# Performance work log

Hardware: AMD Instinct MI355X
Metric: run time of the kernel (lower is better)

The kernel has to match this reference:

```python
import jax, jax.numpy as jnp
import numpy as np


def setup_inputs() -> dict:
    key = jax.random.key(0)
    x = jax.random.normal(key, (4, 3, 8192), dtype=jnp.float32)  # (B, 3, N)
    return {"x": x, "k": 30}


def reference(x, k):
    # x: (B, 3, N)
    x_t = jnp.swapaxes(x, 1, 2)  # (B, N, 3)
    xx = jnp.sum(x_t ** 2, axis=2, keepdims=True)  # (B, N, 1)
    # pairwise squared distances (B, N, N)
    pairwise = xx + jnp.swapaxes(xx, 1, 2) - 2.0 * jnp.matmul(x_t, x)
    # k smallest distances -> negate and take top_k
    _, idx = jax.lax.top_k(-pairwise, k)  # idx: (B, N, k)
    # gather neighbors: (B, N, k, 3)
    neighbors = jax.vmap(lambda pts, i: pts[i])(x_t, idx)
    centroid = jnp.mean(neighbors, axis=2, keepdims=True)  # (B, N, 1, 3)
    centered = neighbors - centroid  # (B, N, k, 3)
    # per-point 3x3 covariance
    cov = jnp.einsum('bnki,bnkj->bnij', centered, centered)  # (B, N, 3, 3)
    _, v = jnp.linalg.eigh(cov)  # eigenvalues ascending
    normals = v[..., :, 0]  # eigenvector of smallest eigenvalue, (B, N, 3)
    # orient normals toward viewpoint (origin): view_dir = -x_t
    dot = jnp.sum(-x_t * normals, axis=-1, keepdims=True)
    normals = jnp.where(dot < 0, -normals, normals)
    x_out = jnp.concatenate([x, jnp.swapaxes(normals, 1, 2)], axis=1)  # (B, 6, N)
    return x_out
```

## Files before the change

### kernel.cpp

```cpp
#include <hip/hip_runtime.h>
#include <math.h>

#define N_PTS   8192
#define KNN     30
#define CAPG    104
#define STR     105
#define GROUPS  8
#define BLOCK   128
#define NZ      64
#define NY      64
#define NBKT    (NZ * NY)
#define CLO     -4.0f
#define CSC     8.0f
#define LAMBDA  48.0f

#define WS_S   0
#define WS_O   524288
#define WS_BS  655360
#define WS_GH  720912
#define WS_GC  786448

__device__ __forceinline__ int clampi(int v, int lo, int hi) {
    return v < lo ? lo : (v > hi ? hi : v);
}
__device__ __forceinline__ int bucket_of(float pz, float py) {
    int zb = clampi((int)floorf((pz - CLO) * CSC), 0, NZ - 1);
    int yb = clampi((int)floorf((py - CLO) * CSC), 0, NY - 1);
    return (zb << 6) | yb;
}

__global__ __launch_bounds__(256) void prep_hist_kernel(const float* __restrict__ x,
                                                        float* __restrict__ out,
                                                        int* __restrict__ ghist) {
    const int i = blockIdx.x * 256 + threadIdx.x;
    const int b = i >> 13;
    const int p = i & (N_PTS - 1);
    const float* xb = x + (size_t)b * 3 * N_PTS;
    float* ob = out + (size_t)b * 6 * N_PTS;
    float px = xb[p], py = xb[N_PTS + p], pz = xb[2 * N_PTS + p];
    ob[p]             = px;
    ob[N_PTS + p]     = py;
    ob[2 * N_PTS + p] = pz;
    atomicAdd(&ghist[(b << 12) + bucket_of(pz, py)], 1);
}

__global__ __launch_bounds__(1024) void prep_scan_kernel(const int* __restrict__ ghist,
                                                         int* __restrict__ bstart,
                                                         int* __restrict__ gcur) {
    __shared__ int wsum[16];
    const int b = blockIdx.x;
    const int t = threadIdx.x;
    const int wid = t >> 6, lane = t & 63;
    const int* gh = ghist + (b << 12);

    int l0 = gh[4 * t], l1 = gh[4 * t + 1], l2 = gh[4 * t + 2], l3 = gh[4 * t + 3];
    int s = l0 + l1 + l2 + l3;
    int sum = s;
    #pragma unroll
    for (int off = 1; off < 64; off <<= 1) {
        int v = __shfl_up(sum, off);
        if (lane >= off) sum += v;
    }
    if (lane == 63) wsum[wid] = sum;
    __syncthreads();
    if (t == 0) {
        int run = 0;
        #pragma unroll
        for (int k = 0; k < 16; ++k) { int v = wsum[k]; wsum[k] = run; run += v; }
    }
    __syncthreads();
    int base = wsum[wid] + (sum - s);
    int b0 = base, b1 = base + l0, b2 = b1 + l1, b3 = b2 + l2;
    int* bsb = bstart + b * (NBKT + 1);
    int* gc  = gcur + (b << 12);
    bsb[4 * t] = b0; bsb[4 * t + 1] = b1; bsb[4 * t + 2] = b2; bsb[4 * t + 3] = b3;
    gc[4 * t]  = b0; gc[4 * t + 1]  = b1; gc[4 * t + 2]  = b2; gc[4 * t + 3]  = b3;
    if (t == 1023) bsb[NBKT] = N_PTS;
}

__global__ __launch_bounds__(256) void prep_scatter_kernel(const float* __restrict__ x,
                                                           float4* __restrict__ S,
                                                           int* __restrict__ O,
                                                           int* __restrict__ gcur) {
    const int i = blockIdx.x * 256 + threadIdx.x;
    const int b = i >> 13;
    const int p = i & (N_PTS - 1);
    const float* xb = x + (size_t)b * 3 * N_PTS;
    float px = xb[p], py = xb[N_PTS + p], pz = xb[2 * N_PTS + p];
    int bk = bucket_of(pz, py);
    int dst = atomicAdd(&gcur[(b << 12) + bk], 1);
    float xx = __fadd_rn(__fadd_rn(__fmul_rn(px, px), __fmul_rn(py, py)),
                         __fmul_rn(pz, pz));
    S[((size_t)b << 13) + dst] = make_float4(px, py, pz, xx);
    O[((size_t)b << 13) + dst] = p;
}

__global__ __launch_bounds__(BLOCK, 6) void knn_normal_kernel(const float4* __restrict__ S,
                                                              const int* __restrict__ O,
                                                              const int* __restrict__ bstart,
                                                              float* __restrict__ out) {
    __shared__ unsigned long long ldk[GROUPS * STR];

    const int t    = threadIdx.x;
    const int l16  = t & 15;
    const int g    = t >> 4;
    const int gsh  = (t & 63) & ~15;
    const int qblk = (blockIdx.x * 1031) & 4095;
    const int qid  = qblk * GROUPS + g;
    const int b    = qid >> 13;
    const int pos  = qid & (N_PTS - 1);
    const float4* __restrict__ P  = S + ((size_t)b << 13);
    const int*    __restrict__ Ob = O + ((size_t)b << 13);
    const int*    __restrict__ bs = bstart + b * (NBKT + 1);
    const float4 qp = P[pos];
    const int    oi = Ob[pos];

    unsigned long long* __restrict__ ldg = ldk + g * STR;

    const float c = fmaxf(sqrtf(qp.w), 1e-3f);
    float rlo = 0.05f, rhi = 6.0f;
    for (int it = 0; it < 12; ++it) {
        float r = 0.5f * (rlo + rhi);
        float slo = fmaxf(c - r, 0.0f);
        float h = (c + r - slo) * 0.125f;
        float f = 0.0f;
        if (l16 <= 8) {
            float sq = slo + h * (float)l16;
            float cs = c - sq;
            float hh = fmaxf(fminf((r * r - cs * cs) * (0.5f / c), 2.0f * sq), 0.0f);
            float w = (l16 == 0 || l16 == 8) ? 1.0f : ((l16 & 1) ? 4.0f : 2.0f);
            f = w * __expf(-0.5f * sq * sq) * sq * hh;
        }
        f += __shfl_xor(f, 1, 16); f += __shfl_xor(f, 2, 16);
        f += __shfl_xor(f, 4, 16); f += __shfl_xor(f, 8, 16);
        float lam = 1089.3f * f * h;
        if (lam < LAMBDA) rlo = r; else rhi = r;
    }
    float rad = rhi * 1.02f;
    float r2  = rad * rad;

    int  cnt = 0;
    bool active = true;

    for (;;) {
        if (active) {
            cnt = 0;
            float w = __fmaf_rn(sqrtf(r2), 1.002f, 1e-3f);
            int zlo = clampi((int)floorf((qp.z - w - CLO) * CSC), 0, NZ - 1);
            int zhi = clampi((int)floorf((qp.z + w - CLO) * CSC), 0, NZ - 1);
            int ylo = clampi((int)floorf((qp.y - w - CLO) * CSC), 0, NY - 1);
            int yhi = clampi((int)floorf((qp.y + w - CLO) * CSC), 0, NY - 1);
            for (int zb = zlo; zb <= zhi; ++zb) {
                int lo = bs[(zb << 6) + ylo];
                int hi = bs[(zb << 6) + yhi + 1];
                int smax = (hi - lo + 31) >> 5;
                for (int s = 0; s < smax; ++s) {
                    int j1  = lo + (s << 5) + l16;
                    int j2  = j1 + 16;
                    int jc1 = j1 < hi ? j1 : hi - 1;
                    int jc2 = j2 < hi ? j2 : hi - 1;
                    float4 p1 = P[jc1];
                    float4 p2 = P[jc2];
                    float mm1 = __fmaf_rn(qp.z, p1.z, __fmaf_rn(qp.y, p1.y, __fmul_rn(qp.x, p1.x)));
                    float d1  = __fsub_rn(__fadd_rn(qp.w, p1.w), __fmul_rn(2.0f, mm1));
                    float mm2 = __fmaf_rn(qp.z, p2.z, __fmaf_rn(qp.y, p2.y, __fmul_rn(qp.x, p2.x)));
                    float d2  = __fsub_rn(__fadd_rn(qp.w, p2.w), __fmul_rn(2.0f, mm2));
                    bool hit1 = (j1 < hi) && (d1 <= r2);
                    bool hit2 = (j2 < hi) && (d2 <= r2);
                    unsigned long long m1 = __ballot(hit1);
                    unsigned sub1 = (unsigned)((m1 >> gsh) & 0xFFFFull);
                    if (hit1) {
                        int slot = cnt + __popc(sub1 & ((1u << l16) - 1u));
                        if (slot < CAPG) {
                            unsigned u = __float_as_uint(d1);
                            u = (u & 0x80000000u) ? ~u : (u | 0x80000000u);
                            ldg[slot] = ((unsigned long long)u << 28) | (unsigned long long)jc1;
                        }
                    }
                    cnt += __popc(sub1);
                    unsigned long long m2 = __ballot(hit2);
                    unsigned sub2 = (unsigned)((m2 >> gsh) & 0xFFFFull);
                    if (hit2) {
                        int slot = cnt + __popc(sub2 & ((1u << l16) - 1u));
                        if (slot < CAPG) {
                            unsigned u = __float_as_uint(d2);
                            u = (u & 0x80000000u) ? ~u : (u | 0x80000000u);
                            ldg[slot] = ((unsigned long long)u << 28) | (unsigned long long)jc2;
                        }
                    }
                    cnt += __popc(sub2);
                }
            }
        }
        bool bad = active && (cnt < KNN || cnt > CAPG);
        if (__ballot(bad) == 0ULL) break;
        active = bad;
        if (active) r2 = (cnt < KNN) ? r2 * 1.6f : r2 * 0.82f;
    }

    unsigned long long k0 = ~0ULL, k1 = ~0ULL, k2 = ~0ULL, k3 = ~0ULL,
                       k4 = ~0ULL, k5 = ~0ULL, k6 = ~0ULL;
    #define FILLK(J, KV) { int idx = l16 + 16 * (J); if (idx < cnt) {            \
        unsigned long long key = ldg[idx];                                       \
        int jc = (int)(key & 0x3FFFull);                                         \
        KV = (key & ~0x0FFFFFFFull) | ((unsigned long long)Ob[jc] << 14)         \
             | (unsigned long long)jc;                                           \
        ldg[idx] = KV; } }
    FILLK(0, k0) FILLK(1, k1) FILLK(2, k2) FILLK(3, k3)
    FILLK(4, k4) FILLK(5, k5) FILLK(6, k6)
    #undef FILLK
    __builtin_amdgcn_wave_barrier();

    int r0 = 0, r1 = 0, r2i = 0, r3 = 0, r4 = 0, r5 = 0, r6 = 0;
    if (cnt <= 64) {
        for (int u = 0; u < cnt; ++u) {
            unsigned long long ku = ldg[u];
            r0 += ku < k0; r1 += ku < k1; r2i += ku < k2; r3 += ku < k3;
        }
        r4 = r5 = r6 = KNN;
    } else {
        for (int u = 0; u < cnt; ++u) {
            unsigned long long ku = ldg[u];
            r0 += ku < k0; r1 += ku < k1; r2i += ku < k2; r3 += ku < k3;
            r4 += ku < k4; r5 += ku < k5; r6 += ku < k6;
        }
    }

    const double qx = (double)qp.x, qy = (double)qp.y, qz = (double)qp.z;
    double sx = 0.0, sy = 0.0, sz = 0.0;
    double sxx = 0.0, sxy = 0.0, sxz = 0.0, syy = 0.0, syz = 0.0, szz = 0.0;

    #define ACCJ(KV, RV) if ((RV) < KNN) {                                       \
        float4 p = P[(int)((KV) & 0x3FFFull)];                                   \
        double ax = (double)p.x - qx, ay = (double)p.y - qy, az = (double)p.z - qz; \
        sx += ax; sy += ay; sz += az;                                            \
        sxx = fma(ax, ax, sxx); sxy = fma(ax, ay, sxy); sxz = fma(ax, az, sxz);  \
        syy = fma(ay, ay, syy); syz = fma(ay, az, syz); szz = fma(az, az, szz); }
    ACCJ(k0, r0) ACCJ(k1, r1) ACCJ(k2, r2i) ACCJ(k3, r3)
    ACCJ(k4, r4) ACCJ(k5, r5) ACCJ(k6, r6)
    #undef ACCJ

    #pragma unroll
    for (int off = 1; off < 16; off <<= 1) {
        sx  += __shfl_xor(sx,  off, 16); sy  += __shfl_xor(sy,  off, 16); sz  += __shfl_xor(sz,  off, 16);
        sxx += __shfl_xor(sxx, off, 16); sxy += __shfl_xor(sxy, off, 16); sxz += __shfl_xor(sxz, off, 16);
        syy += __shfl_xor(syy, off, 16); syz += __shfl_xor(syz, off, 16); szz += __shfl_xor(szz, off, 16);
    }

    if (l16 == 0) {
        const double kinv = 1.0 / (double)KNN;
        double m00 = sxx - sx * sx * kinv;
        double m11 = syy - sy * sy * kinv;
        double m22 = szz - sz * sz * kinv;
        double m01 = sxy - sx * sy * kinv;
        double m02 = sxz - sx * sz * kinv;
        double m12 = syz - sy * sz * kinv;

        double nx = 1.0, ny = 0.0, nz = 0.0;
        double q3 = (m00 + m11 + m22) / 3.0;
        double p1 = m01 * m01 + m02 * m02 + m12 * m12;
        double d00 = m00 - q3, d11 = m11 - q3, d22 = m22 - q3;
        double p2 = d00 * d00 + d11 * d11 + d22 * d22 + 2.0 * p1;
        if (p2 > 1e-280) {
            double pp = sqrt(p2 / 6.0);
            double ip = 1.0 / pp;
            double b00 = d00 * ip, b11 = d11 * ip, b22 = d22 * ip;
            double b01 = m01 * ip, b02 = m02 * ip, b12 = m12 * ip;
            double detB = b00 * (b11 * b22 - b12 * b12)
                        - b01 * (b01 * b22 - b12 * b02)
                        + b02 * (b01 * b12 - b11 * b02);
            double rr = 0.5 * detB;
            rr = rr < -1.0 ? -1.0 : (rr > 1.0 ? 1.0 : rr);
            double phi = acos(rr) / 3.0;
            double lam = q3 + 2.0 * pp * cos(phi + 2.0943951023931953);
            double a00 = m00 - lam, a11 = m11 - lam, a22 = m22 - lam;
            double v0x = m01 * m12 - m02 * a11, v0y = m02 * m01 - a00 * m12, v0z = a00 * a11 - m01 * m01;
            double v1x = m01 * a22 - m02 * m12, v1y = m02 * m02 - a00 * a22, v1z = a00 * m12 - m01 * m02;
            double v2x = a11 * a22 - m12 * m12, v2y = m12 * m02 - m01 * a22, v2z = m01 * m12 - a11 * m02;
            double n0 = v0x * v0x + v0y * v0y + v0z * v0z;
            double n1 = v1x * v1x + v1y * v1y + v1z * v1z;
            double n2 = v2x * v2x + v2y * v2y + v2z * v2z;
            double bx = v0x, by = v0y, bz = v0z, bn = n0;
            if (n1 > bn) { bx = v1x; by = v1y; bz = v1z; bn = n1; }
            if (n2 > bn) { bx = v2x; by = v2y; bz = v2z; bn = n2; }
            if (bn > 1e-280) {
                double inv = 1.0 / sqrt(bn);
                nx = bx * inv; ny = by * inv; nz = bz * inv;
            }
        }
        double dq = -(qx * nx + qy * ny + qz * nz);
        if (dq < 0.0) { nx = -nx; ny = -ny; nz = -nz; }

        float* ob = out + (size_t)b * 6 * N_PTS;
        ob[3 * N_PTS + oi] = (float)nx;
        ob[4 * N_PTS + oi] = (float)ny;
        ob[5 * N_PTS + oi] = (float)nz;
    }
}

extern "C" void kernel_launch(void* const* d_in, const int* in_sizes, int n_in,
                              void* d_out, int out_size, void* d_ws, size_t ws_size,
                              hipStream_t stream) {
    const float* x = (const float*)d_in[0];
    float* out = (float*)d_out;
    char* ws = (char*)d_ws;
    float4* S    = (float4*)(ws + WS_S);
    int*    O    = (int*)(ws + WS_O);
    int*    bsta = (int*)(ws + WS_BS);
    int*    gh   = (int*)(ws + WS_GH);
    int*    gc   = (int*)(ws + WS_GC);

    hipMemsetAsync(gh, 0, 4 * NBKT * sizeof(int), stream);
    prep_hist_kernel   <<<dim3(128), dim3(256),  0, stream>>>(x, out, gh);
    prep_scan_kernel   <<<dim3(4),   dim3(1024), 0, stream>>>(gh, bsta, gc);
    prep_scatter_kernel<<<dim3(128), dim3(256),  0, stream>>>(x, S, O, gc);
    knn_normal_kernel  <<<dim3(32768 / GROUPS), dim3(BLOCK), 0, stream>>>(S, O, bsta, out);
}
```

Measured before the change: 170.9 us.

## Defer heavy KNN queries to a separate full-wave kernel

Before searching, each query estimates how many candidates its bucket window holds. Queries above a threshold are appended to a global list and handled by a second kernel that uses a full 64-lane wave per query instead of 16 lanes. This targets load imbalance, where a few dense queries hold up their waves. The bisection now runs 14 iterations instead of 12, and the unrolled fixed-register rank selection is replaced by a strided loop with a block-wide __syncthreads. The change adds an atomic-append pass, an extra kernel launch and a memset, and the deferred-list workspace reuses the region used by the histogram buffers.

```diff
diff --git a/kernel.cpp b/kernel.cpp
--- a/kernel.cpp
+++ b/kernel.cpp
@@ -13,12 +13,16 @@
 #define CLO     -4.0f
 #define CSC     8.0f
 #define LAMBDA  48.0f
+#define THRESH  1024
+#define HGRID   2048
 
 #define WS_S   0
 #define WS_O   524288
 #define WS_BS  655360
 #define WS_GH  720912
 #define WS_GC  786448
+#define WS_DL  720912
+#define WS_DC  851984
 
 __device__ __forceinline__ int clampi(int v, int lo, int hi) {
     return v < lo ? lo : (v > hi ? hi : v);
@@ -27,6 +31,81 @@
     int zb = clampi((int)floorf((pz - CLO) * CSC), 0, NZ - 1);
     int yb = clampi((int)floorf((py - CLO) * CSC), 0, NY - 1);
     return (zb << 6) | yb;
+}
+
+__device__ __forceinline__ float solve_r2(float qw, int l16) {
+    const float c = fmaxf(sqrtf(qw), 1e-3f);
+    float rlo = 0.05f, rhi = 6.0f;
+    for (int it = 0; it < 14; ++it) {
+        float r = 0.5f * (rlo + rhi);
+        float slo = fmaxf(c - r, 0.0f);
+        float h = (c + r - slo) * 0.125f;
+        float f = 0.0f;
+        if (l16 <= 8) {
+            float sq = slo + h * (float)l16;
+            float cs = c - sq;
+            float hh = fmaxf(fminf((r * r - cs * cs) * (0.5f / c), 2.0f * sq), 0.0f);
+            float w = (l16 == 0 || l16 == 8) ? 1.0f : ((l16 & 1) ? 4.0f : 2.0f);
+            f = w * __expf(-0.5f * sq * sq) * sq * hh;
+        }
+        f += __shfl_xor(f, 1, 16); f += __shfl_xor(f, 2, 16);
+        f += __shfl_xor(f, 4, 16); f += __shfl_xor(f, 8, 16);
+        float lam = 1089.3f * f * h;
+        if (lam < LAMBDA) rlo = r; else rhi = r;
+    }
+    float rad = rhi * 1.02f;
+    return rad * rad;
+}
+
+__device__ __forceinline__ void normal_epilogue(double sx, double sy, double sz,
+        double sxx, double sxy, double sxz, double syy, double syz, double szz,
+        double qx, double qy, double qz, float* ob, int oi) {
+    const double kinv = 1.0 / (double)KNN;
+    double m00 = sxx - sx * sx * kinv;
+    double m11 = syy - sy * sy * kinv;
+    double m22 = szz - sz * sz * kinv;
+    double m01 = sxy - sx * sy * kinv;
+    double m02 = sxz - sx * sz * kinv;
+    double m12 = syz - sy * sz * kinv;
+
+    double nx = 1.0, ny = 0.0, nz = 0.0;
+    double q3 = (m00 + m11 + m22) / 3.0;
+    double p1 = m01 * m01 + m02 * m02 + m12 * m12;
+    double d00 = m00 - q3, d11 = m11 - q3, d22 = m22 - q3;
+    double p2 = d00 * d00 + d11 * d11 + d22 * d22 + 2.0 * p1;
+    if (p2 > 1e-280) {
+        double pp = sqrt(p2 / 6.0);
+        double ip = 1.0 / pp;
+        double b00 = d00 * ip, b11 = d11 * ip, b22 = d22 * ip;
+        double b01 = m01 * ip, b02 = m02 * ip, b12 = m12 * ip;
+        double detB = b00 * (b11 * b22 - b12 * b12)
+                    - b01 * (b01 * b22 - b12 * b02)
+                    + b02 * (b01 * b12 - b11 * b02);
+        double rr = 0.5 * detB;
+        rr = rr < -1.0 ? -1.0 : (rr > 1.0 ? 1.0 : rr);
+        double phi = acos(rr) / 3.0;
+        double lam = q3 + 2.0 * pp * cos(phi + 2.0943951023931953);
+        double a00 = m00 - lam, a11 = m11 - lam, a22 = m22 - lam;
+        double v0x = m01 * m12 - m02 * a11, v0y = m02 * m01 - a00 * m12, v0z = a00 * a11 - m01 * m01;
+        double v1x = m01 * a22 - m02 * m12, v1y = m02 * m02 - a00 * a22, v1z = a00 * m12 - m01 * m02;
+        double v2x = a11 * a22 - m12 * m12, v2y = m12 * m02 - m01 * a22, v2z = m01 * m12 - a11 * m02;
+        double n0 = v0x * v0x + v0y * v0y + v0z * v0z;
+        double n1 = v1x * v1x + v1y * v1y + v1z * v1z;
+        double n2 = v2x * v2x + v2y * v2y + v2z * v2z;
+        double bx = v0x, by = v0y, bz = v0z, bn = n0;
+        if (n1 > bn) { bx = v1x; by = v1y; bz = v1z; bn = n1; }
+        if (n2 > bn) { bx = v2x; by = v2y; bz = v2z; bn = n2; }
+        if (bn > 1e-280) {
+            double inv = 1.0 / sqrt(bn);
+            nx = bx * inv; ny = by * inv; nz = bz * inv;
+        }
+    }
+    double dq = -(qx * nx + qy * ny + qz * nz);
+    if (dq < 0.0) { nx = -nx; ny = -ny; nz = -nz; }
+
+    ob[3 * N_PTS + oi] = (float)nx;
+    ob[4 * N_PTS + oi] = (float)ny;
+    ob[5 * N_PTS + oi] = (float)nz;
 }
 
 __global__ __launch_bounds__(256) void prep_hist_kernel(const float* __restrict__ x,
@@ -98,6 +177,8 @@
 __global__ __launch_bounds__(BLOCK, 6) void knn_normal_kernel(const float4* __restrict__ S,
                                                               const int* __restrict__ O,
                                                               const int* __restrict__ bstart,
+                                                              int* __restrict__ dlist,
+                                                              int* __restrict__ dcount,
                                                               float* __restrict__ out) {
     __shared__ unsigned long long ldk[GROUPS * STR];
 
@@ -117,30 +198,27 @@
 
     unsigned long long* __restrict__ ldg = ldk + g * STR;
 
-    const float c = fmaxf(sqrtf(qp.w), 1e-3f);
-    float rlo = 0.05f, rhi = 6.0f;
-    for (int it = 0; it < 12; ++it) {
-        float r = 0.5f * (rlo + rhi);
-        float slo = fmaxf(c - r, 0.0f);
-        float h = (c + r - slo) * 0.125f;
-        float f = 0.0f;
-        if (l16 <= 8) {
-            float sq = slo + h * (float)l16;
-            float cs = c - sq;
-            float hh = fmaxf(fminf((r * r - cs * cs) * (0.5f / c), 2.0f * sq), 0.0f);
-            float w = (l16 == 0 || l16 == 8) ? 1.0f : ((l16 & 1) ? 4.0f : 2.0f);
-            f = w * __expf(-0.5f * sq * sq) * sq * hh;
-        }
-        f += __shfl_xor(f, 1, 16); f += __shfl_xor(f, 2, 16);
-        f += __shfl_xor(f, 4, 16); f += __shfl_xor(f, 8, 16);
-        float lam = 1089.3f * f * h;
-        if (lam < LAMBDA) rlo = r; else rhi = r;
-    }
-    float rad = rhi * 1.02f;
-    float r2  = rad * rad;
+    float r2 = solve_r2(qp.w, l16);
+
+    bool defer;
+    {
+        float w = __fmaf_rn(sqrtf(r2), 1.002f, 1e-3f);
+        int zlo = clampi((int)floorf((qp.z - w - CLO) * CSC), 0, NZ - 1);
+        int zhi = clampi((int)floorf((qp.z + w - CLO) * CSC), 0, NZ - 1);
+        int ylo = clampi((int)floorf((qp.y - w - CLO) * CSC), 0, NY - 1);
+        int yhi = clampi((int)floorf((qp.y + w - CLO) * CSC), 0, NY - 1);
+        int tot = 0;
+        for (int zb = zlo; zb <= zhi; ++zb)
+            tot += bs[(zb << 6) + yhi + 1] - bs[(zb << 6) + ylo];
+        defer = tot > THRESH;
+    }
+    if (defer && l16 == 0) {
+        int slot = atomicAdd(dcount, 1);
+        dlist[slot] = qid;
+    }
 
     int  cnt = 0;
-    bool active = true;
+    bool active = !defer;
 
     for (;;) {
         if (active) {
@@ -198,47 +276,29 @@
         if (active) r2 = (cnt < KNN) ? r2 * 1.6f : r2 * 0.82f;
     }
 
-    unsigned long long k0 = ~0ULL, k1 = ~0ULL, k2 = ~0ULL, k3 = ~0ULL,
-                       k4 = ~0ULL, k5 = ~0ULL, k6 = ~0ULL;
-    #define FILLK(J, KV) { int idx = l16 + 16 * (J); if (idx < cnt) {            \
-        unsigned long long key = ldg[idx];                                       \
-        int jc = (int)(key & 0x3FFFull);                                         \
-        KV = (key & ~0x0FFFFFFFull) | ((unsigned long long)Ob[jc] << 14)         \
-             | (unsigned long long)jc;                                           \
-        ldg[idx] = KV; } }
-    FILLK(0, k0) FILLK(1, k1) FILLK(2, k2) FILLK(3, k3)
-    FILLK(4, k4) FILLK(5, k5) FILLK(6, k6)
-    #undef FILLK
-    __builtin_amdgcn_wave_barrier();
-
-    int r0 = 0, r1 = 0, r2i = 0, r3 = 0, r4 = 0, r5 = 0, r6 = 0;
-    if (cnt <= 64) {
-        for (int u = 0; u < cnt; ++u) {
-            unsigned long long ku = ldg[u];
-            r0 += ku < k0; r1 += ku < k1; r2i += ku < k2; r3 += ku < k3;
-        }
-        r4 = r5 = r6 = KNN;
-    } else {
-        for (int u = 0; u < cnt; ++u) {
-            unsigned long long ku = ldg[u];
-            r0 += ku < k0; r1 += ku < k1; r2i += ku < k2; r3 += ku < k3;
-            r4 += ku < k4; r5 += ku < k5; r6 += ku < k6;
-        }
-    }
+    for (int k = l16; k < cnt; k += 16) {
+        unsigned long long key = ldg[k];
+        int jc = (int)(key & 0x3FFFull);
+        ldg[k] = (key & ~0x0FFFFFFFull) | ((unsigned long long)Ob[jc] << 14) | (unsigned long long)jc;
+    }
+    __syncthreads();
 
     const double qx = (double)qp.x, qy = (double)qp.y, qz = (double)qp.z;
     double sx = 0.0, sy = 0.0, sz = 0.0;
     double sxx = 0.0, sxy = 0.0, sxz = 0.0, syy = 0.0, syz = 0.0, szz = 0.0;
 
-    #define ACCJ(KV, RV) if ((RV) < KNN) {                                       \
-        float4 p = P[(int)((KV) & 0x3FFFull)];                                   \
-        double ax = (double)p.x - qx, ay = (double)p.y - qy, az = (double)p.z - qz; \
-        sx += ax; sy += ay; sz += az;                                            \
-        sxx = fma(ax, ax, sxx); sxy = fma(ax, ay, sxy); sxz = fma(ax, az, sxz);  \
-        syy = fma(ay, ay, syy); syz = fma(ay, az, syz); szz = fma(az, az, szz); }
-    ACCJ(k0, r0) ACCJ(k1, r1) ACCJ(k2, r2i) ACCJ(k3, r3)
-    ACCJ(k4, r4) ACCJ(k5, r5) ACCJ(k6, r6)
-    #undef ACCJ
+    for (int k = l16; k < cnt; k += 16) {
+        unsigned long long key = ldg[k];
+        int rank = 0;
+        for (int u = 0; u < cnt; ++u) rank += (ldg[u] < key) ? 1 : 0;
+        if (rank < KNN) {
+            float4 p = P[(int)(key & 0x3FFFull)];
+            double ax = (double)p.x - qx, ay = (double)p.y - qy, az = (double)p.z - qz;
+            sx += ax; sy += ay; sz += az;
+            sxx = fma(ax, ax, sxx); sxy = fma(ax, ay, sxy); sxz = fma(ax, az, sxz);
+            syy = fma(ay, ay, syy); syz = fma(ay, az, syz); szz = fma(az, az, szz);
+        }
+    }
 
     #pragma unroll
     for (int off = 1; off < 16; off <<= 1) {
@@ -247,54 +307,122 @@
         syy += __shfl_xor(syy, off, 16); syz += __shfl_xor(syz, off, 16); szz += __shfl_xor(szz, off, 16);
     }
 
-    if (l16 == 0) {
-        const double kinv = 1.0 / (double)KNN;
-        double m00 = sxx - sx * sx * kinv;
-        double m11 = syy - sy * sy * kinv;
-        double m22 = szz - sz * sz * kinv;
-        double m01 = sxy - sx * sy * kinv;
-        double m02 = sxz - sx * sz * kinv;
-        double m12 = syz - sy * sz * kinv;
-
-        double nx = 1.0, ny = 0.0, nz = 0.0;
-        double q3 = (m00 + m11 + m22) / 3.0;
-        double p1 = m01 * m01 + m02 * m02 + m12 * m12;
-        double d00 = m00 - q3, d11 = m11 - q3, d22 = m22 - q3;
-        double p2 = d00 * d00 + d11 * d11 + d22 * d22 + 2.0 * p1;
-        if (p2 > 1e-280) {
-            double pp = sqrt(p2 / 6.0);
-            double ip = 1.0 / pp;
-            double b00 = d00 * ip, b11 = d11 * ip, b22 = d22 * ip;
-            double b01 = m01 * ip, b02 = m02 * ip, b12 = m12 * ip;
-            double detB = b00 * (b11 * b22 - b12 * b12)
-                        - b01 * (b01 * b22 - b12 * b02)
-                        + b02 * (b01 * b12 - b11 * b02);
-            double rr = 0.5 * detB;
-            rr = rr < -1.0 ? -1.0 : (rr > 1.0 ? 1.0 : rr);
-            double phi = acos(rr) / 3.0;
-            double lam = q3 + 2.0 * pp * cos(phi + 2.0943951023931953);
-            double a00 = m00 - lam, a11 = m11 - lam, a22 = m22 - lam;
-            double v0x = m01 * m12 - m02 * a11, v0y = m02 * m01 - a00 * m12, v0z = a00 * a11 - m01 * m01;
-            double v1x = m01 * a22 - m02 * m12, v1y = m02 * m02 - a00 * a22, v1z = a00 * m12 - m01 * m02;
-            double v2x = a11 * a22 - m12 * m12, v2y = m12 * m02 - m01 * a22, v2z = m01 * m12 - a11 * m02;
-            double n0 = v0x * v0x + v0y * v0y + v0z * v0z;
-            double n1 = v1x * v1x + v1y * v1y + v1z * v1z;
-            double n2 = v2x * v2x + v2y * v2y + v2z * v2z;
-            double bx = v0x, by = v0y, bz = v0z, bn = n0;
-            if (n1 > bn) { bx = v1x; by = v1y; bz = v1z; bn = n1; }
-            if (n2 > bn) { bx = v2x; by = v2y; bz = v2z; bn = n2; }
-            if (bn > 1e-280) {
-                double inv = 1.0 / sqrt(bn);
-                nx = bx * inv; ny = by * inv; nz = bz * inv;
+    if (l16 == 0 && !defer) {
+        float* ob = out + (size_t)b * 6 * N_PTS;
+        normal_epilogue(sx, sy, sz, sxx, sxy, sxz, syy, syz, szz, qx, qy, qz, ob, oi);
+    }
+}
+
+__global__ __launch_bounds__(64) void knn_heavy_kernel(const float4* __restrict__ S,
+                                                       const int* __restrict__ O,
+                                                       const int* __restrict__ bstart,
+                                                       const int* __restrict__ dlist,
+                                                       const int* __restrict__ dcount,
+                                                       float* __restrict__ out) {
+    __shared__ unsigned long long ldg[STR];
+    const int lane = threadIdx.x;
+    const int l16  = lane & 15;
+    const int nd   = *dcount;
+
+    for (int qi = blockIdx.x; qi < nd; qi += HGRID) {
+        const int qid = dlist[qi];
+        const int b   = qid >> 13;
+        const int pos = qid & (N_PTS - 1);
+        const float4* __restrict__ P  = S + ((size_t)b << 13);
+        const int*    __restrict__ Ob = O + ((size_t)b << 13);
+        const int*    __restrict__ bs = bstart + b * (NBKT + 1);
+        const float4 qp = P[pos];
+        const int    oi = Ob[pos];
+
+        float r2 = solve_r2(qp.w, l16);
+        int cnt = 0;
+
+        for (;;) {
+            cnt = 0;
+            float w = __fmaf_rn(sqrtf(r2), 1.002f, 1e-3f);
+            int zlo = clampi((int)floorf((qp.z - w - CLO) * CSC), 0, NZ - 1);
+            int zhi = clampi((int)floorf((qp.z + w - CLO) * CSC), 0, NZ - 1);
+            int ylo = clampi((int)floorf((qp.y - w - CLO) * CSC), 0, NY - 1);
+            int yhi = clampi((int)floorf((qp.y + w - CLO) * CSC), 0, NY - 1);
+            for (int zb = zlo; zb <= zhi; ++zb) {
+                int lo = bs[(zb << 6) + ylo];
+                int hi = bs[(zb << 6) + yhi + 1];
+                int smax = (hi - lo + 127) >> 7;
+                for (int s = 0; s < smax; ++s) {
+                    int j1  = lo + (s << 7) + lane;
+                    int j2  = j1 + 64;
+                    int jc1 = j1 < hi ? j1 : hi - 1;
+                    int jc2 = j2 < hi ? j2 : hi - 1;
+                    float4 p1 = P[jc1];
+                    float4 p2 = P[jc2];
+                    float mm1 = __fmaf_rn(qp.z, p1.z, __fmaf_rn(qp.y, p1.y, __fmul_rn(qp.x, p1.x)));
+                    float d1  = __fsub_rn(__fadd_rn(qp.w, p1.w), __fmul_rn(2.0f, mm1));
+                    float mm2 = __fmaf_rn(qp.z, p2.z, __fmaf_rn(qp.y, p2.y, __fmul_rn(qp.x, p2.x)));
+                    float d2  = __fsub_rn(__fadd_rn(qp.w, p2.w), __fmul_rn(2.0f, mm2));
+                    bool hit1 = (j1 < hi) && (d1 <= r2);
+                    bool hit2 = (j2 < hi) && (d2 <= r2);
+                    unsigned long long m1 = __ballot(hit1);
+                    if (hit1) {
+                        int slot = cnt + __popcll(m1 & ((1ull << lane) - 1ull));
+                        if (slot < CAPG) {
+                            unsigned u = __float_as_uint(d1);
+                            u = (u & 0x80000000u) ? ~u : (u | 0x80000000u);
+                            ldg[slot] = ((unsigned long long)u << 28) | (unsigned long long)jc1;
+                        }
+                    }
+                    cnt += __popcll(m1);
+                    unsigned long long m2 = __ballot(hit2);
+                    if (hit2) {
+                        int slot = cnt + __popcll(m2 & ((1ull << lane) - 1ull));
+                        if (slot < CAPG) {
+                            unsigned u = __float_as_uint(d2);
+                            u = (u & 0x80000000u) ? ~u : (u | 0x80000000u);
+                            ldg[slot] = ((unsigned long long)u << 28) | (unsigned long long)jc2;
+                        }
+                    }
+                    cnt += __popcll(m2);
+                }
             }
-        }
-        double dq = -(qx * nx + qy * ny + qz * nz);
-        if (dq < 0.0) { nx = -nx; ny = -ny; nz = -nz; }
-
-        float* ob = out + (size_t)b * 6 * N_PTS;
-        ob[3 * N_PTS + oi] = (float)nx;
-        ob[4 * N_PTS + oi] = (float)ny;
-        ob[5 * N_PTS + oi] = (float)nz;
+            if (cnt >= KNN && cnt <= CAPG) break;
+            r2 = (cnt < KNN) ? r2 * 1.6f : r2 * 0.82f;
+        }
+
+        for (int k = lane; k < cnt; k += 64) {
+            unsigned long long key = ldg[k];
+            int jc = (int)(key & 0x3FFFull);
+            ldg[k] = (key & ~0x0FFFFFFFull) | ((unsigned long long)Ob[jc] << 14) | (unsigned long long)jc;
+        }
+        __syncthreads();
+
+        const double qx = (double)qp.x, qy = (double)qp.y, qz = (double)qp.z;
+        double sx = 0.0, sy = 0.0, sz = 0.0;
+        double sxx = 0.0, sxy = 0.0, sxz = 0.0, syy = 0.0, syz = 0.0, szz = 0.0;
+
+        for (int k = lane; k < cnt; k += 64) {
+            unsigned long long key = ldg[k];
+            int rank = 0;
+            for (int u = 0; u < cnt; ++u) rank += (ldg[u] < key) ? 1 : 0;
+            if (rank < KNN) {
+                float4 p = P[(int)(key & 0x3FFFull)];
+                double ax = (double)p.x - qx, ay = (double)p.y - qy, az = (double)p.z - qz;
+                sx += ax; sy += ay; sz += az;
+                sxx = fma(ax, ax, sxx); sxy = fma(ax, ay, sxy); sxz = fma(ax, az, sxz);
+                syy = fma(ay, ay, syy); syz = fma(ay, az, syz); szz = fma(az, az, szz);
+            }
+        }
+
+        #pragma unroll
+        for (int off = 1; off < 64; off <<= 1) {
+            sx  += __shfl_xor(sx,  off, 64); sy  += __shfl_xor(sy,  off, 64); sz  += __shfl_xor(sz,  off, 64);
+            sxx += __shfl_xor(sxx, off, 64); sxy += __shfl_xor(sxy, off, 64); sxz += __shfl_xor(sxz, off, 64);
+            syy += __shfl_xor(syy, off, 64); syz += __shfl_xor(syz, off, 64); szz += __shfl_xor(szz, off, 64);
+        }
+
+        if (lane == 0) {
+            float* ob = out + (size_t)b * 6 * N_PTS;
+            normal_epilogue(sx, sy, sz, sxx, sxy, sxz, syy, syz, szz, qx, qy, qz, ob, oi);
+        }
+        __syncthreads();
     }
 }
 
@@ -309,10 +437,14 @@
     int*    bsta = (int*)(ws + WS_BS);
     int*    gh   = (int*)(ws + WS_GH);
     int*    gc   = (int*)(ws + WS_GC);
+    int*    dl   = (int*)(ws + WS_DL);
+    int*    dc   = (int*)(ws + WS_DC);
 
     hipMemsetAsync(gh, 0, 4 * NBKT * sizeof(int), stream);
+    hipMemsetAsync(dc, 0, sizeof(int), stream);
     prep_hist_kernel   <<<dim3(128), dim3(256),  0, stream>>>(x, out, gh);
     prep_scan_kernel   <<<dim3(4),   dim3(1024), 0, stream>>>(gh, bsta, gc);
     prep_scatter_kernel<<<dim3(128), dim3(256),  0, stream>>>(x, S, O, gc);
-    knn_normal_kernel  <<<dim3(32768 / GROUPS), dim3(BLOCK), 0, stream>>>(S, O, bsta, out);
-}
+    knn_normal_kernel  <<<dim3(32768 / GROUPS), dim3(BLOCK), 0, stream>>>(S, O, bsta, dl, dc, out);
+    knn_heavy_kernel   <<<dim3(HGRID), dim3(64), 0, stream>>>(S, O, bsta, dl, dc, out);
+}
```

Result: slower. 211.2 us (+23.6%).
